# Kernel optimization log

Measured on AMD Instinct MI355X. Metric: run time of the kernel, lower is better.

## Reference

```python
import jax, jax.numpy as jnp
import numpy as np

B = 32          # decode batch (one query token per sequence)
HID = 4096      # hidden_size
H = 32          # num_heads
D = 128         # head_dim
BLK = 16        # KV-cache block size (vLLM default)
MAXB = 64       # max blocks per sequence
NBLK = 2048     # total cache blocks
S = MAXB * BLK  # max context length = 1024
ROPE_THETA = 10000.0


def _rope(x, positions):
    # x: [B, H, D], positions: [B] int. GPT-NeoX / Llama half-split rotary.
    half = D // 2
    inv_freq = 1.0 / (ROPE_THETA ** (jnp.arange(0, half, dtype=jnp.float32) / half))
    freqs = positions.astype(jnp.float32)[:, None] * inv_freq[None, :]  # [B, D/2]
    cos = jnp.cos(freqs)[:, None, :]  # [B, 1, D/2]
    sin = jnp.sin(freqs)[:, None, :]
    x1, x2 = x[..., :half], x[..., half:]
    return jnp.concatenate([x1 * cos - x2 * sin, x1 * sin + x2 * cos], axis=-1)


def setup_inputs() -> dict:
    key = jax.random.key(0)
    ks = jax.random.split(key, 8)
    hidden_states = jax.random.normal(ks[0], (B, HID), jnp.float32)
    Wq = jax.random.normal(ks[1], (HID, HID), jnp.float32) * 0.02
    Wk = jax.random.normal(ks[2], (HID, HID), jnp.float32) * 0.02
    Wv = jax.random.normal(ks[3], (HID, HID), jnp.float32) * 0.02
    Wo = jax.random.normal(ks[4], (HID, HID), jnp.float32) * 0.02
    k_cache = jax.random.normal(ks[5], (NBLK, BLK, H, D), jnp.float32)
    v_cache = jax.random.normal(ks[6], (NBLK, BLK, H, D), jnp.float32)
    # each sequence owns MAXB distinct cache blocks (non-contiguous)
    block_tables = jax.random.permutation(ks[7], NBLK)[: B * MAXB].reshape(B, MAXB).astype(jnp.int32)
    context_lens = jax.random.randint(jax.random.fold_in(key, 9), (B,), S // 2, S + 1).astype(jnp.int32)
    positions = context_lens - 1  # current token position
    slot_mapping = (block_tables[jnp.arange(B), positions // BLK] * BLK + positions % BLK).astype(jnp.int32)
    return dict(hidden_states=hidden_states, k_cache=k_cache, v_cache=v_cache,
                Wq=Wq, Wk=Wk, Wv=Wv, Wo=Wo,
                positions=positions, slot_mapping=slot_mapping,
                block_tables=block_tables, context_lens=context_lens)


def reference(hidden_states, k_cache, v_cache, Wq, Wk, Wv, Wo,
              positions, slot_mapping, block_tables, context_lens):
    # QKV projections (bias-free, torch Linear convention: x @ W.T)
    q = (hidden_states @ Wq.T).reshape(B, H, D)
    k = (hidden_states @ Wk.T).reshape(B, H, D)
    v = (hidden_states @ Wv.T).reshape(B, H, D)
    q = _rope(q, positions)
    k = _rope(k, positions)
    # write new k/v into the paged cache at slot_mapping
    kc = k_cache.reshape(NBLK * BLK, H, D).at[slot_mapping].set(k)
    vc = v_cache.reshape(NBLK * BLK, H, D).at[slot_mapping].set(v)
    kc = kc.reshape(NBLK, BLK, H, D)
    vc = vc.reshape(NBLK, BLK, H, D)
    # paged gather: [B, MAXB, BLK, H, D] -> [B, S, H, D]
    keys = kc[block_tables].reshape(B, S, H, D)
    vals = vc[block_tables].reshape(B, S, H, D)
    scores = jnp.einsum('bhd,bshd->bhs', q, keys) * (D ** -0.5)
    valid = jnp.arange(S)[None, :] < context_lens[:, None]  # [B, S]
    scores = jnp.where(valid[:, None, :], scores, jnp.float32(-1e30))
    probs = jax.nn.softmax(scores, axis=-1)
    attn = jnp.einsum('bhs,bshd->bhd', probs, vals).reshape(B, H * D)
    return attn @ Wo.T
```

## Files before the change

### kernel.cpp

```cpp
#include <hip/hip_runtime.h>
#include <math.h>

#define HID 4096
#define B 32
#define H 32
#define D 128
#define KBLK 16
#define MAXB 64
#define S_MAX 1024
#define CHUNK 256
#define NCHUNK 4

__global__ __launch_bounds__(256) void gemv_kernel(
    const float* __restrict__ W0, const float* __restrict__ W1, const float* __restrict__ W2,
    const float* __restrict__ x, float* __restrict__ out)
{
    __shared__ float wt[8][256];
    const int bid = blockIdx.x;
    const int mat = bid >> 9;
    const int n0 = (bid & 511) << 3;
    const float* W = (mat == 0) ? W0 : ((mat == 1) ? W1 : W2);
    float* outp = out + (size_t)mat * (B * HID);

    const int tid = threadIdx.x;
    const int lane = tid & 63;
    const int wid = tid >> 6;
    const int b0 = wid << 3;

    float acc[8][8];
#pragma unroll
    for (int c = 0; c < 8; ++c)
#pragma unroll
        for (int j = 0; j < 8; ++j) acc[c][j] = 0.f;

    for (int k0 = 0; k0 < HID; k0 += 256) {
        __syncthreads();
#pragma unroll
        for (int i = 0; i < 2; ++i) {
            int idx = tid + i * 256;
            int row = idx >> 6;
            int c4 = idx & 63;
            float4 v = *reinterpret_cast<const float4*>(
                &W[(size_t)(n0 + row) * HID + k0 + (c4 << 2)]);
            *reinterpret_cast<float4*>(&wt[row][c4 << 2]) = v;
        }
        __syncthreads();

        float4 hs4[8];
#pragma unroll
        for (int j = 0; j < 8; ++j)
            hs4[j] = *reinterpret_cast<const float4*>(
                &x[(size_t)(b0 + j) * HID + k0 + (lane << 2)]);

#pragma unroll
        for (int c = 0; c < 8; ++c) {
            float4 w4 = *reinterpret_cast<const float4*>(&wt[c][lane << 2]);
#pragma unroll
            for (int j = 0; j < 8; ++j) {
                acc[c][j] += w4.x * hs4[j].x;
                acc[c][j] += w4.y * hs4[j].y;
                acc[c][j] += w4.z * hs4[j].z;
                acc[c][j] += w4.w * hs4[j].w;
            }
        }
    }

#pragma unroll
    for (int m = 1; m < 64; m <<= 1) {
#pragma unroll
        for (int c = 0; c < 8; ++c)
#pragma unroll
            for (int j = 0; j < 8; ++j)
                acc[c][j] += __shfl_xor(acc[c][j], m, 64);
    }
    float myval = 0.f;
#pragma unroll
    for (int c = 0; c < 8; ++c)
#pragma unroll
        for (int j = 0; j < 8; ++j)
            myval = (lane == (c * 8 + j)) ? acc[c][j] : myval;
    const int oc = lane >> 3;
    const int oj = lane & 7;
    outp[(size_t)(b0 + oj) * HID + n0 + oc] = myval;
}

__global__ __launch_bounds__(64) void rope_kernel(float* __restrict__ qkv,
                                                  const int* __restrict__ positions)
{
    const int bh = blockIdx.x;
    const int b = bh >> 5;
    const int h = bh & 31;
    const int d = threadIdx.x;
    const float pos = (float)positions[b];
    const float inv = exp2f(-(float)d * 0.20762050593046013f);
    const float f = pos * inv;
    const float cs = cosf(f);
    const float sn = sinf(f);
#pragma unroll
    for (int mat = 0; mat < 2; ++mat) {
        float* base = qkv + (size_t)mat * (B * HID) + (size_t)b * HID + h * D;
        float x1 = base[d];
        float x2 = base[d + 64];
        base[d] = x1 * cs - x2 * sn;
        base[d + 64] = x1 * sn + x2 * cs;
    }
}

__global__ __launch_bounds__(256) void attn_partial_kernel(
    const float* __restrict__ qkv,
    const float* __restrict__ k_cache,
    const float* __restrict__ v_cache,
    const int* __restrict__ block_tables,
    const int* __restrict__ context_lens,
    const int* __restrict__ positions,
    float* __restrict__ pm,
    float* __restrict__ pl,
    float* __restrict__ po)
{
    const int h = blockIdx.x;
    const int c = blockIdx.y;
    const int b = blockIdx.z;
    const int L = context_lens[b];
    const int s0 = c << 8;
    if (s0 >= L) return;
    const int Lc = min(L - s0, CHUNK);
    const int pos = positions[b];
    const int tid = threadIdx.x;

    __shared__ float sc[CHUNK];
    __shared__ float red[8];
    __shared__ int btl[16];
    __shared__ float o4[4][D];

    if (tid < 16) btl[tid] = block_tables[b * MAXB + (c << 4) + tid];
    __syncthreads();

    const float* qptr = qkv + (size_t)b * HID + h * D;
    const float* knew = qkv + (size_t)(B * HID) + (size_t)b * HID + h * D;
    const float* vnew = qkv + (size_t)(2 * B * HID) + (size_t)b * HID + h * D;
    const float scale = 0.088388347648318447f;

    const int hw = tid >> 5;
    const int hl = tid & 31;
    const float4 qv = *reinterpret_cast<const float4*>(qptr + (hl << 2));

    int i = hw;
    for (; i + 8 < Lc; i += 16) {
        const int sA = s0 + i, sB = s0 + i + 8;
        const float* kp0 = (sA == pos) ? knew
            : k_cache + ((size_t)(btl[i >> 4] * KBLK + (sA & 15)) * H + h) * D;
        const float* kp1 = (sB == pos) ? knew
            : k_cache + ((size_t)(btl[(i + 8) >> 4] * KBLK + (sB & 15)) * H + h) * D;
        float4 k0 = *reinterpret_cast<const float4*>(kp0 + (hl << 2));
        float4 k1 = *reinterpret_cast<const float4*>(kp1 + (hl << 2));
        float d0 = qv.x * k0.x + qv.y * k0.y + qv.z * k0.z + qv.w * k0.w;
        float d1 = qv.x * k1.x + qv.y * k1.y + qv.z * k1.z + qv.w * k1.w;
#pragma unroll
        for (int m = 16; m; m >>= 1) {
            d0 += __shfl_xor(d0, m, 64);
            d1 += __shfl_xor(d1, m, 64);
        }
        if (hl == 0) { sc[i] = d0 * scale; sc[i + 8] = d1 * scale; }
    }
    for (; i < Lc; i += 8) {
        const int sA = s0 + i;
        const float* kp = (sA == pos) ? knew
            : k_cache + ((size_t)(btl[i >> 4] * KBLK + (sA & 15)) * H + h) * D;
        float4 k0 = *reinterpret_cast<const float4*>(kp + (hl << 2));
        float d0 = qv.x * k0.x + qv.y * k0.y + qv.z * k0.z + qv.w * k0.w;
#pragma unroll
        for (int m = 16; m; m >>= 1) d0 += __shfl_xor(d0, m, 64);
        if (hl == 0) sc[i] = d0 * scale;
    }
    for (; i < CHUNK; i += 8)
        if (hl == 0) sc[i] = -1e30f;
    __syncthreads();

    const int w = tid >> 6;
    const float x = sc[tid];
    float m = x;
#pragma unroll
    for (int mm = 32; mm; mm >>= 1) m = fmaxf(m, __shfl_xor(m, mm, 64));
    if ((tid & 63) == 0) red[w] = m;
    __syncthreads();
    const float gm = fmaxf(fmaxf(red[0], red[1]), fmaxf(red[2], red[3]));

    float p = (x > -1e29f) ? __expf(x - gm) : 0.f;
    sc[tid] = p;
    float l = p;
#pragma unroll
    for (int mm = 32; mm; mm >>= 1) l += __shfl_xor(l, mm, 64);
    if ((tid & 63) == 0) red[4 + w] = l;
    __syncthreads();
    const float gl = red[4] + red[5] + red[6] + red[7];

    const int l2 = (tid & 63) << 1;
    float accx = 0.f, accy = 0.f;
    i = w;
    for (; i + 4 < Lc; i += 8) {
        const int sA = s0 + i, sB = s0 + i + 4;
        const float* vp0 = (sA == pos) ? vnew
            : v_cache + ((size_t)(btl[i >> 4] * KBLK + (sA & 15)) * H + h) * D;
        const float* vp1 = (sB == pos) ? vnew
            : v_cache + ((size_t)(btl[(i + 4) >> 4] * KBLK + (sB & 15)) * H + h) * D;
        float2 v0 = *reinterpret_cast<const float2*>(vp0 + l2);
        float2 v1 = *reinterpret_cast<const float2*>(vp1 + l2);
        float p0 = sc[i], p1 = sc[i + 4];
        accx += p0 * v0.x; accy += p0 * v0.y;
        accx += p1 * v1.x; accy += p1 * v1.y;
    }
    for (; i < Lc; i += 4) {
        const float* vp = (s0 + i == pos) ? vnew
            : v_cache + ((size_t)(btl[i >> 4] * KBLK + ((s0 + i) & 15)) * H + h) * D;
        float2 v0 = *reinterpret_cast<const float2*>(vp + l2);
        float p0 = sc[i];
        accx += p0 * v0.x; accy += p0 * v0.y;
    }
    o4[w][l2] = accx;
    o4[w][l2 + 1] = accy;
    __syncthreads();

    const int bh = b * H + h;
    if (tid < D) {
        float o = o4[0][tid] + o4[1][tid] + o4[2][tid] + o4[3][tid];
        po[((size_t)bh * NCHUNK + c) * D + tid] = o;
    } else if (tid == D) {
        pm[bh * NCHUNK + c] = gm;
        pl[bh * NCHUNK + c] = gl;
    }
}

__global__ __launch_bounds__(128) void attn_combine_kernel(
    const float* __restrict__ pm, const float* __restrict__ pl,
    const float* __restrict__ po, const int* __restrict__ context_lens,
    float* __restrict__ attn_out)
{
    const int bh = blockIdx.x;
    const int b = bh >> 5;
    const int tid = threadIdx.x;
    const int nc = (context_lens[b] + CHUNK - 1) >> 8;

    float m = -1e30f;
    for (int c = 0; c < nc; ++c) m = fmaxf(m, pm[bh * NCHUNK + c]);
    float wsum = 0.f, o = 0.f;
    for (int c = 0; c < nc; ++c) {
        float wc = __expf(pm[bh * NCHUNK + c] - m);
        wsum += wc * pl[bh * NCHUNK + c];
        o += wc * po[((size_t)bh * NCHUNK + c) * D + tid];
    }
    attn_out[(size_t)bh * D + tid] = o / wsum;
}

extern "C" void kernel_launch(void* const* d_in, const int* in_sizes, int n_in,
                              void* d_out, int out_size, void* d_ws, size_t ws_size,
                              hipStream_t stream) {
    const float* hs        = (const float*)d_in[0];
    const float* k_cache   = (const float*)d_in[1];
    const float* v_cache   = (const float*)d_in[2];
    const float* Wq        = (const float*)d_in[3];
    const float* Wk        = (const float*)d_in[4];
    const float* Wv        = (const float*)d_in[5];
    const float* Wo        = (const float*)d_in[6];
    const int*   positions = (const int*)d_in[7];
    const int*   block_tables = (const int*)d_in[9];
    const int*   context_lens = (const int*)d_in[10];
    float* out = (float*)d_out;

    float* qkv     = (float*)d_ws;
    float* attn_ws = qkv + (size_t)3 * B * HID;
    float* pm      = attn_ws + (size_t)B * HID;
    float* pl      = pm + (size_t)B * H * NCHUNK;
    float* po      = pl + (size_t)B * H * NCHUNK;

    gemv_kernel<<<dim3(3 * 512), 256, 0, stream>>>(Wq, Wk, Wv, hs, qkv);
    rope_kernel<<<dim3(B * H), 64, 0, stream>>>(qkv, positions);
    attn_partial_kernel<<<dim3(H, NCHUNK, B), 256, 0, stream>>>(
        qkv, k_cache, v_cache, block_tables, context_lens, positions, pm, pl, po);
    attn_combine_kernel<<<dim3(B * H), 128, 0, stream>>>(pm, pl, po, context_lens, attn_ws);
    gemv_kernel<<<dim3(512), 256, 0, stream>>>(Wo, Wo, Wo, attn_ws, out);
}
```

Before: 267.3 us.

## Fuse RoPE into QKV GEMV epilogue, use LDS reduction, unroll attention loops

The RoPE kernel is folded into the QKV GEMV. Each block of the Q/K projections now loads the rotary pair rows (d and d+64) of one head, so rotation can be applied in registers before the store. The final 64-lane shuffle reduction is replaced by a transpose through shared memory followed by a short 3-step shuffle, which cuts shuffle count. The K and V loops in the attention kernel are unrolled to four rows per iteration to keep more loads in flight, at the cost of more registers and extra shared memory.

Measured after the change: 262.5 us. No clear change (-1.8%).

```diff
diff --git a/kernel.cpp b/kernel.cpp
--- a/kernel.cpp
+++ b/kernel.cpp
@@ -7,18 +7,22 @@
 #define D 128
 #define KBLK 16
 #define MAXB 64
-#define S_MAX 1024
 #define CHUNK 256
 #define NCHUNK 4
 
+template <int MODE>
 __global__ __launch_bounds__(256) void gemv_kernel(
     const float* __restrict__ W0, const float* __restrict__ W1, const float* __restrict__ W2,
-    const float* __restrict__ x, float* __restrict__ out)
+    const float* __restrict__ x, const int* __restrict__ positions, float* __restrict__ out)
 {
     __shared__ float wt[8][256];
+    __shared__ float buf[4][8][66];
     const int bid = blockIdx.x;
-    const int mat = bid >> 9;
-    const int n0 = (bid & 511) << 3;
+    const int mat = (MODE == 0) ? (bid >> 9) : 0;
+    const int sub = bid & 511;
+    const bool rope = (MODE == 0) && (mat < 2);
+    const int head = sub >> 4;
+    const int p0 = (sub & 15) << 2;
     const float* W = (mat == 0) ? W0 : ((mat == 1) ? W1 : W2);
     float* outp = out + (size_t)mat * (B * HID);
 
@@ -37,12 +41,14 @@
         __syncthreads();
 #pragma unroll
         for (int i = 0; i < 2; ++i) {
-            int idx = tid + i * 256;
-            int row = idx >> 6;
+            int idx = tid + (i << 8);
+            int r = idx >> 6;
             int c4 = idx & 63;
+            int cr = rope ? (head * 128 + p0 + (r & 3) + ((r >> 2) << 6))
+                          : ((sub << 3) + r);
             float4 v = *reinterpret_cast<const float4*>(
-                &W[(size_t)(n0 + row) * HID + k0 + (c4 << 2)]);
-            *reinterpret_cast<float4*>(&wt[row][c4 << 2]) = v;
+                &W[(size_t)cr * HID + k0 + (c4 << 2)]);
+            *reinterpret_cast<float4*>(&wt[r][c4 << 2]) = v;
         }
         __syncthreads();
 
@@ -65,45 +71,48 @@
         }
     }
 
-#pragma unroll
-    for (int m = 1; m < 64; m <<= 1) {
-#pragma unroll
-        for (int c = 0; c < 8; ++c)
-#pragma unroll
-            for (int j = 0; j < 8; ++j)
-                acc[c][j] += __shfl_xor(acc[c][j], m, 64);
-    }
-    float myval = 0.f;
-#pragma unroll
-    for (int c = 0; c < 8; ++c)
-#pragma unroll
-        for (int j = 0; j < 8; ++j)
-            myval = (lane == (c * 8 + j)) ? acc[c][j] : myval;
-    const int oc = lane >> 3;
-    const int oj = lane & 7;
-    outp[(size_t)(b0 + oj) * HID + n0 + oc] = myval;
-}
-
-__global__ __launch_bounds__(64) void rope_kernel(float* __restrict__ qkv,
-                                                  const int* __restrict__ positions)
-{
-    const int bh = blockIdx.x;
-    const int b = bh >> 5;
-    const int h = bh & 31;
-    const int d = threadIdx.x;
-    const float pos = (float)positions[b];
-    const float inv = exp2f(-(float)d * 0.20762050593046013f);
-    const float f = pos * inv;
-    const float cs = cosf(f);
-    const float sn = sinf(f);
-#pragma unroll
-    for (int mat = 0; mat < 2; ++mat) {
-        float* base = qkv + (size_t)mat * (B * HID) + (size_t)b * HID + h * D;
-        float x1 = base[d];
-        float x2 = base[d + 64];
-        base[d] = x1 * cs - x2 * sn;
-        base[d + 64] = x1 * sn + x2 * cs;
-    }
+    float res[8];
+#pragma unroll
+    for (int c = 0; c < 8; ++c) {
+#pragma unroll
+        for (int j = 0; j < 8; ++j) buf[wid][j][lane] = acc[c][j];
+        __builtin_amdgcn_sched_barrier(0);
+        const float* rp = &buf[wid][lane >> 3][(lane & 7) << 3];
+        float4 a = *reinterpret_cast<const float4*>(rp);
+        float4 bb = *reinterpret_cast<const float4*>(rp + 4);
+        __builtin_amdgcn_sched_barrier(0);
+        float s = ((a.x + a.y) + (a.z + a.w)) + ((bb.x + bb.y) + (bb.z + bb.w));
+        s += __shfl_xor(s, 1, 64);
+        s += __shfl_xor(s, 2, 64);
+        s += __shfl_xor(s, 4, 64);
+        res[c] = s;
+    }
+
+    const int jme = lane >> 3;
+    const int cme = lane & 7;
+    float myv;
+    if (rope) {
+        const float pf = (float)positions[b0 + jme];
+        float ro[8];
+#pragma unroll
+        for (int cc = 0; cc < 4; ++cc) {
+            float invf = exp2f(-(float)(p0 + cc) * 0.20762050593046013f);
+            float f = pf * invf;
+            float cs = cosf(f), sn = sinf(f);
+            ro[cc]     = res[cc] * cs - res[cc + 4] * sn;
+            ro[cc + 4] = res[cc] * sn + res[cc + 4] * cs;
+        }
+        myv = ro[0];
+#pragma unroll
+        for (int cc = 1; cc < 8; ++cc) myv = (cme == cc) ? ro[cc] : myv;
+    } else {
+        myv = res[0];
+#pragma unroll
+        for (int cc = 1; cc < 8; ++cc) myv = (cme == cc) ? res[cc] : myv;
+    }
+    const int colw = rope ? (head * 128 + p0 + (cme & 3) + ((cme >> 2) << 6))
+                          : ((sub << 3) + cme);
+    outp[(size_t)(b0 + jme) * HID + colw] = myv;
 }
 
 __global__ __launch_bounds__(256) void attn_partial_kernel(
@@ -145,22 +154,35 @@
     const float4 qv = *reinterpret_cast<const float4*>(qptr + (hl << 2));
 
     int i = hw;
-    for (; i + 8 < Lc; i += 16) {
-        const int sA = s0 + i, sB = s0 + i + 8;
+    for (; i + 24 < Lc; i += 32) {
+        const int sA = s0 + i, sB = sA + 8, sC = sA + 16, sD = sA + 24;
         const float* kp0 = (sA == pos) ? knew
             : k_cache + ((size_t)(btl[i >> 4] * KBLK + (sA & 15)) * H + h) * D;
         const float* kp1 = (sB == pos) ? knew
             : k_cache + ((size_t)(btl[(i + 8) >> 4] * KBLK + (sB & 15)) * H + h) * D;
+        const float* kp2 = (sC == pos) ? knew
+            : k_cache + ((size_t)(btl[(i + 16) >> 4] * KBLK + (sC & 15)) * H + h) * D;
+        const float* kp3 = (sD == pos) ? knew
+            : k_cache + ((size_t)(btl[(i + 24) >> 4] * KBLK + (sD & 15)) * H + h) * D;
         float4 k0 = *reinterpret_cast<const float4*>(kp0 + (hl << 2));
         float4 k1 = *reinterpret_cast<const float4*>(kp1 + (hl << 2));
+        float4 k2 = *reinterpret_cast<const float4*>(kp2 + (hl << 2));
+        float4 k3 = *reinterpret_cast<const float4*>(kp3 + (hl << 2));
         float d0 = qv.x * k0.x + qv.y * k0.y + qv.z * k0.z + qv.w * k0.w;
         float d1 = qv.x * k1.x + qv.y * k1.y + qv.z * k1.z + qv.w * k1.w;
+        float d2 = qv.x * k2.x + qv.y * k2.y + qv.z * k2.z + qv.w * k2.w;
+        float d3 = qv.x * k3.x + qv.y * k3.y + qv.z * k3.z + qv.w * k3.w;
 #pragma unroll
         for (int m = 16; m; m >>= 1) {
             d0 += __shfl_xor(d0, m, 64);
             d1 += __shfl_xor(d1, m, 64);
-        }
-        if (hl == 0) { sc[i] = d0 * scale; sc[i + 8] = d1 * scale; }
+            d2 += __shfl_xor(d2, m, 64);
+            d3 += __shfl_xor(d3, m, 64);
+        }
+        if (hl == 0) {
+            sc[i] = d0 * scale; sc[i + 8] = d1 * scale;
+            sc[i + 16] = d2 * scale; sc[i + 24] = d3 * scale;
+        }
     }
     for (; i < Lc; i += 8) {
         const int sA = s0 + i;
@@ -177,15 +199,15 @@
     __syncthreads();
 
     const int w = tid >> 6;
-    const float x = sc[tid];
-    float m = x;
+    const float xv = sc[tid];
+    float m = xv;
 #pragma unroll
     for (int mm = 32; mm; mm >>= 1) m = fmaxf(m, __shfl_xor(m, mm, 64));
     if ((tid & 63) == 0) red[w] = m;
     __syncthreads();
     const float gm = fmaxf(fmaxf(red[0], red[1]), fmaxf(red[2], red[3]));
 
-    float p = (x > -1e29f) ? __expf(x - gm) : 0.f;
+    float p = (xv > -1e29f) ? __expf(xv - gm) : 0.f;
     sc[tid] = p;
     float l = p;
 #pragma unroll
@@ -197,17 +219,25 @@
     const int l2 = (tid & 63) << 1;
     float accx = 0.f, accy = 0.f;
     i = w;
-    for (; i + 4 < Lc; i += 8) {
-        const int sA = s0 + i, sB = s0 + i + 4;
+    for (; i + 12 < Lc; i += 16) {
+        const int sA = s0 + i, sB = sA + 4, sC = sA + 8, sD = sA + 12;
         const float* vp0 = (sA == pos) ? vnew
             : v_cache + ((size_t)(btl[i >> 4] * KBLK + (sA & 15)) * H + h) * D;
         const float* vp1 = (sB == pos) ? vnew
             : v_cache + ((size_t)(btl[(i + 4) >> 4] * KBLK + (sB & 15)) * H + h) * D;
+        const float* vp2 = (sC == pos) ? vnew
+            : v_cache + ((size_t)(btl[(i + 8) >> 4] * KBLK + (sC & 15)) * H + h) * D;
+        const float* vp3 = (sD == pos) ? vnew
+            : v_cache + ((size_t)(btl[(i + 12) >> 4] * KBLK + (sD & 15)) * H + h) * D;
         float2 v0 = *reinterpret_cast<const float2*>(vp0 + l2);
         float2 v1 = *reinterpret_cast<const float2*>(vp1 + l2);
-        float p0 = sc[i], p1 = sc[i + 4];
+        float2 v2 = *reinterpret_cast<const float2*>(vp2 + l2);
+        float2 v3 = *reinterpret_cast<const float2*>(vp3 + l2);
+        float p0 = sc[i], p1 = sc[i + 4], p2 = sc[i + 8], p3 = sc[i + 12];
         accx += p0 * v0.x; accy += p0 * v0.y;
         accx += p1 * v1.x; accy += p1 * v1.y;
+        accx += p2 * v2.x; accy += p2 * v2.y;
+        accx += p3 * v3.x; accy += p3 * v3.y;
     }
     for (; i < Lc; i += 4) {
         const float* vp = (s0 + i == pos) ? vnew
@@ -272,10 +302,9 @@
     float* pl      = pm + (size_t)B * H * NCHUNK;
     float* po      = pl + (size_t)B * H * NCHUNK;
 
-    gemv_kernel<<<dim3(3 * 512), 256, 0, stream>>>(Wq, Wk, Wv, hs, qkv);
-    rope_kernel<<<dim3(B * H), 64, 0, stream>>>(qkv, positions);
+    gemv_kernel<0><<<dim3(3 * 512), 256, 0, stream>>>(Wq, Wk, Wv, hs, positions, qkv);
     attn_partial_kernel<<<dim3(H, NCHUNK, B), 256, 0, stream>>>(
         qkv, k_cache, v_cache, block_tables, context_lens, positions, pm, pl, po);
     attn_combine_kernel<<<dim3(B * H), 128, 0, stream>>>(pm, pl, po, context_lens, attn_ws);
-    gemv_kernel<<<dim3(512), 256, 0, stream>>>(Wo, Wo, Wo, attn_ws, out);
+    gemv_kernel<1><<<dim3(512), 256, 0, stream>>>(Wo, Wo, Wo, attn_ws, positions, out);
 }
```
